# Performance work log

Hardware: AMD Instinct MI355X
Metric: run time of the kernel (lower is better)

The kernel has to match this reference:

```python
import jax, jax.numpy as jnp
import numpy as np

D_MODEL = 2048
N_HEADS = 16
N_KV_HEADS = 4
D_K = D_MODEL // N_HEADS          # 128
N_REP = N_HEADS // N_KV_HEADS     # 4
MAX_SEQ_LEN = 2048


def _rope_tables():
    # Matches torch Rotary: d_k//4 geometric freqs followed by d_k//4 zeros.
    freqs = (1.0 / 10000.0) ** jnp.linspace(0.0, 1.0, D_K // 4, dtype=jnp.float32)
    freqs = jnp.concatenate([freqs, jnp.zeros(D_K // 4, dtype=jnp.float32)])
    t = jnp.arange(MAX_SEQ_LEN, dtype=jnp.float32)
    theta = t[:, None] * freqs[None, :]          # [max_seq_len, d_k//2]
    return jnp.cos(theta), jnp.sin(theta)


def _apply_rotary(x, cos, sin):
    # Faithful to original: x is (B, H, T, D) and the table is indexed by
    # x.size(-3) == H (the original code rotates per-HEAD, broadcast over time).
    H = x.shape[1]
    c = cos[None, :H, None, :]
    s = sin[None, :H, None, :]
    xf = x.astype(jnp.float32)
    x1, x2 = jnp.split(xf, 2, axis=-1)
    y1 = x1 * c + x2 * s
    y2 = -x1 * s + x2 * c
    return jnp.concatenate([y1, y2], axis=-1).astype(x.dtype)


def setup_inputs() -> dict:
    key = jax.random.key(0)
    ks = jax.random.split(key, 5)
    B, T = 2, 2048
    scale = 1.0 / np.sqrt(D_MODEL)
    x = jax.random.normal(ks[0], (B, T, D_MODEL), dtype=jnp.float32)
    wq = jax.random.normal(ks[1], (N_HEADS * D_K, D_MODEL), dtype=jnp.float32) * scale
    wk = jax.random.normal(ks[2], (N_KV_HEADS * D_K, D_MODEL), dtype=jnp.float32) * scale
    wv = jax.random.normal(ks[3], (N_KV_HEADS * D_K, D_MODEL), dtype=jnp.float32) * scale
    wo = jax.random.normal(ks[4], (D_MODEL, D_MODEL), dtype=jnp.float32) * scale
    return {"x": x, "wq": wq, "wk": wk, "wv": wv, "wo": wo}


def reference(x, wq, wk, wv, wo):
    B, T, _ = x.shape
    cos, sin = _rope_tables()

    Q = (x @ wq.T).reshape(B, T, N_HEADS, D_K).transpose(0, 2, 1, 3)      # (B,Hq,T,D)
    K = (x @ wk.T).reshape(B, T, N_KV_HEADS, D_K).transpose(0, 2, 1, 3)   # (B,Hkv,T,D)
    V = (x @ wv.T).reshape(B, T, N_KV_HEADS, D_K).transpose(0, 2, 1, 3)

    Q = _apply_rotary(Q, cos, sin)
    K = _apply_rotary(K, cos, sin)

    # repeat_interleave over head dim to match query heads
    K = jnp.repeat(K, N_REP, axis=1)   # (B,Hq,T,D)
    V = jnp.repeat(V, N_REP, axis=1)

    scale = 1.0 / jnp.sqrt(jnp.asarray(D_K, dtype=jnp.float32))
    scores = jnp.einsum('bhqd,bhkd->bhqk', Q, K) * scale
    causal = jnp.tril(jnp.ones((T, T), dtype=bool))
    scores = jnp.where(causal[None, None, :, :], scores, jnp.finfo(scores.dtype).min)
    attn = jax.nn.softmax(scores, axis=-1)
    out = jnp.einsum('bhqk,bhkd->bhqd', attn, V)          # (B,Hq,T,D)
    out = out.transpose(0, 2, 1, 3).reshape(B, T, D_MODEL)
    return out @ wo.T
```

## Files before the change

### kernel.cpp

```cpp
#include <hip/hip_runtime.h>
#include <cstdint>
#include <cstddef>

typedef __attribute__((ext_vector_type(8))) short bf16x8;
typedef __attribute__((ext_vector_type(4))) float f32x4;
typedef __attribute__((ext_vector_type(16))) float f32x16;
typedef unsigned short ushort_t;

#define MFMA_BF16(a, b, c) __builtin_amdgcn_mfma_f32_16x16x32_bf16((a), (b), (c), 0, 0, 0)
#define MFMA32_BF16(a, b, c) __builtin_amdgcn_mfma_f32_32x32x16_bf16((a), (b), (c), 0, 0, 0)

__device__ __forceinline__ unsigned short f2bf(float f) {
  unsigned int u = __float_as_uint(f);
  u += 0x7fffu + ((u >> 16) & 1u);
  return (unsigned short)(u >> 16);
}
__device__ __forceinline__ float bf2f(unsigned short h) {
  return __uint_as_float(((unsigned int)h) << 16);
}
__device__ __forceinline__ float exp2_fast(float x) {
  float r;
  asm("v_exp_f32 %0, %1" : "=v"(r) : "v"(x));
  return r;
}
__device__ __forceinline__ uint32_t cvtpk_bf16(float lo, float hi) {
  uint32_t r;
  asm("v_cvt_pk_bf16_f32 %0, %1, %2" : "=v"(r) : "v"(lo), "v"(hi));
  return r;
}

__device__ __forceinline__ void gload_lds16(const void* g, void* lds) {
  __builtin_amdgcn_global_load_lds(
      (const __attribute__((address_space(1))) void*)g,
      (__attribute__((address_space(3))) void*)lds, 16, 0, 0);
}

__global__ __launch_bounds__(256)
void cvt_kernel(const float* __restrict__ x, const float* __restrict__ wq,
                const float* __restrict__ wk, const float* __restrict__ wv,
                const float* __restrict__ wo,
                ushort_t* __restrict__ xb, ushort_t* __restrict__ wqb,
                ushort_t* __restrict__ wkb, ushort_t* __restrict__ wvb,
                ushort_t* __restrict__ wob) {
  const float* src; ushort_t* dst; int n;
  switch (blockIdx.y) {
    case 0:  src = x;  dst = xb;  n = 8388608; break;
    case 1:  src = wq; dst = wqb; n = 4194304; break;
    case 2:  src = wk; dst = wkb; n = 1048576; break;
    case 3:  src = wv; dst = wvb; n = 1048576; break;
    default: src = wo; dst = wob; n = 4194304; break;
  }
  const int i = (int)(blockIdx.x * 256u + threadIdx.x) * 4;
  if (i >= n) return;
  const float4 v = *(const float4*)(src + i);
  union { unsigned short us[4]; unsigned long long u64; } pk;
  pk.us[0] = f2bf(v.x); pk.us[1] = f2bf(v.y);
  pk.us[2] = f2bf(v.z); pk.us[3] = f2bf(v.w);
  *(unsigned long long*)(dst + i) = pk.u64;
}

__global__ __launch_bounds__(256, 2)
void gemm_qkv(const ushort_t* __restrict__ A,
              const ushort_t* __restrict__ WQ, const ushort_t* __restrict__ WK,
              const ushort_t* __restrict__ WV,
              ushort_t* __restrict__ Qb, ushort_t* __restrict__ Kb,
              ushort_t* __restrict__ Vtb) {
  __shared__ bf16x8 smem_v[4096];
  char* smem = (char*)smem_v;
  const int tid  = threadIdx.x;
  const int lane = tid & 63;
  const int wave = tid >> 6;
  const int wr = wave >> 1, wc = wave & 1;
  const int y = blockIdx.y;
  int mode, ylocal;
  const ushort_t* Bsel;
  if (y < 16)      { mode = 0; ylocal = y;      Bsel = WQ; }
  else if (y < 20) { mode = 1; ylocal = y - 16; Bsel = WK; }
  else             { mode = 2; ylocal = y - 20; Bsel = WV; }
  const ushort_t* Abase = A + (size_t)blockIdx.x * 128 * 2048;
  const ushort_t* Bbase = Bsel + (size_t)ylocal * 128 * 2048;

  f32x4 acc[4][4] = {};

  #pragma unroll
  for (int it = 0; it < 4; ++it) {
    const int chunk = it * 4 + wave;
    const int r  = chunk * 8 + (lane >> 3);
    const int cg = (lane & 7) ^ (r & 7);
    gload_lds16(Abase + (size_t)r * 2048 + cg * 8, smem + chunk * 1024);
    gload_lds16(Bbase + (size_t)r * 2048 + cg * 8, smem + 16384 + chunk * 1024);
  }
  __syncthreads();

  for (int t = 0; t < 32; ++t) {
    if (t + 1 < 32) {
      char* dst = smem + ((t + 1) & 1) * 32768;
      const int k0 = (t + 1) * 64;
      #pragma unroll
      for (int it = 0; it < 4; ++it) {
        const int chunk = it * 4 + wave;
        const int r  = chunk * 8 + (lane >> 3);
        const int cg = (lane & 7) ^ (r & 7);
        gload_lds16(Abase + (size_t)r * 2048 + k0 + cg * 8, dst + chunk * 1024);
        gload_lds16(Bbase + (size_t)r * 2048 + k0 + cg * 8, dst + 16384 + chunk * 1024);
      }
    }

    char* As = smem + (t & 1) * 32768;
    char* Bs = As + 16384;
    bf16x8 af[2][4], bf_[2][4];
    #pragma unroll
    for (int kki = 0; kki < 2; ++kki) {
      #pragma unroll
      for (int m = 0; m < 4; ++m) {
        const int row = wr * 64 + m * 16 + (lane & 15);
        const int cg  = ((kki << 2) + (lane >> 4)) ^ (row & 7);
        af[kki][m] = *(const bf16x8*)(As + row * 128 + cg * 16);
      }
      #pragma unroll
      for (int n = 0; n < 4; ++n) {
        const int row = wc * 64 + n * 16 + (lane & 15);
        const int cg  = ((kki << 2) + (lane >> 4)) ^ (row & 7);
        bf_[kki][n] = *(const bf16x8*)(Bs + row * 128 + cg * 16);
      }
    }
    #pragma unroll
    for (int kki = 0; kki < 2; ++kki)
      #pragma unroll
      for (int m = 0; m < 4; ++m)
        #pragma unroll
        for (int n = 0; n < 4; ++n)
          acc[m][n] = MFMA_BF16(af[kki][m], bf_[kki][n], acc[m][n]);

    __syncthreads();
  }

  const int row0 = blockIdx.x * 128 + wr * 64;
  const int col0 = ylocal * 128 + wc * 64;
  #pragma unroll
  for (int m = 0; m < 4; ++m) {
    #pragma unroll
    for (int n = 0; n < 4; ++n) {
      #pragma unroll
      for (int j = 0; j < 4; ++j) {
        const int gm = row0 + m * 16 + ((lane >> 4) << 2) + j;
        const int gn = col0 + n * 16 + (lane & 15);
        const float v = acc[m][n][j];
        if (mode == 0) {
          Qb[(size_t)gm * 2048 + gn] = f2bf(v);
        } else if (mode == 1) {
          Kb[(size_t)gm * 512 + gn] = f2bf(v);
        } else {
          const int bb = gm >> 11, t2 = gm & 2047;
          Vtb[(size_t)bb * 512 * 2048 + (size_t)gn * 2048 + t2] = f2bf(v);
        }
      }
    }
  }
}

template<int WMODE>
__global__ __launch_bounds__(256, 2)
void gemm_bt(const ushort_t* __restrict__ A, const ushort_t* __restrict__ B,
             void* __restrict__ Cout, int M, int N, int K) {
  __shared__ bf16x8 smem_v[4096];
  char* smem = (char*)smem_v;
  const int tid  = threadIdx.x;
  const int lane = tid & 63;
  const int wave = tid >> 6;
  const int wr = wave >> 1, wc = wave & 1;
  const ushort_t* Abase = A + (size_t)blockIdx.x * 128 * K;
  const ushort_t* Bbase = B + (size_t)blockIdx.y * 128 * K;

  f32x4 acc[4][4] = {};
  const int nk = K >> 6;

  #pragma unroll
  for (int it = 0; it < 4; ++it) {
    const int chunk = it * 4 + wave;
    const int r  = chunk * 8 + (lane >> 3);
    const int cg = (lane & 7) ^ (r & 7);
    gload_lds16(Abase + (size_t)r * K + cg * 8, smem + chunk * 1024);
    gload_lds16(Bbase + (size_t)r * K + cg * 8, smem + 16384 + chunk * 1024);
  }
  __syncthreads();

  for (int t = 0; t < nk; ++t) {
    if (t + 1 < nk) {
      char* dst = smem + ((t + 1) & 1) * 32768;
      const int k0 = (t + 1) * 64;
      #pragma unroll
      for (int it = 0; it < 4; ++it) {
        const int chunk = it * 4 + wave;
        const int r  = chunk * 8 + (lane >> 3);
        const int cg = (lane & 7) ^ (r & 7);
        gload_lds16(Abase + (size_t)r * K + k0 + cg * 8, dst + chunk * 1024);
        gload_lds16(Bbase + (size_t)r * K + k0 + cg * 8, dst + 16384 + chunk * 1024);
      }
    }

    char* As = smem + (t & 1) * 32768;
    char* Bs = As + 16384;
    bf16x8 af[2][4], bf_[2][4];
    #pragma unroll
    for (int kki = 0; kki < 2; ++kki) {
      #pragma unroll
      for (int m = 0; m < 4; ++m) {
        const int row = wr * 64 + m * 16 + (lane & 15);
        const int cg  = ((kki << 2) + (lane >> 4)) ^ (row & 7);
        af[kki][m] = *(const bf16x8*)(As + row * 128 + cg * 16);
      }
      #pragma unroll
      for (int n = 0; n < 4; ++n) {
        const int row = wc * 64 + n * 16 + (lane & 15);
        const int cg  = ((kki << 2) + (lane >> 4)) ^ (row & 7);
        bf_[kki][n] = *(const bf16x8*)(Bs + row * 128 + cg * 16);
      }
    }
    #pragma unroll
    for (int kki = 0; kki < 2; ++kki)
      #pragma unroll
      for (int m = 0; m < 4; ++m)
        #pragma unroll
        for (int n = 0; n < 4; ++n)
          acc[m][n] = MFMA_BF16(af[kki][m], bf_[kki][n], acc[m][n]);

    __syncthreads();
  }

  const int row0 = blockIdx.x * 128 + wr * 64;
  const int col0 = blockIdx.y * 128 + wc * 64;
  #pragma unroll
  for (int m = 0; m < 4; ++m) {
    #pragma unroll
    for (int n = 0; n < 4; ++n) {
      #pragma unroll
      for (int j = 0; j < 4; ++j) {
        const int gm = row0 + m * 16 + ((lane >> 4) << 2) + j;
        const int gn = col0 + n * 16 + (lane & 15);
        const float v = acc[m][n][j];
        if (WMODE == 0) {
          ((ushort_t*)Cout)[(size_t)gm * N + gn] = f2bf(v);
        } else if (WMODE == 1) {
          ((float*)Cout)[(size_t)gm * N + gn] = v;
        } else {
          const int bb = gm >> 11, t2 = gm & 2047;
          ((ushort_t*)Cout)[(size_t)bb * N * 2048 + (size_t)gn * 2048 + t2] = f2bf(v);
        }
      }
    }
  }
}

__global__ __launch_bounds__(256)
void rope_k_kernel(ushort_t* __restrict__ K) {
  const int idx = blockIdx.x * 256 + threadIdx.x;
  const int NK = 4096 * 4 * 32;
  if (idx >= NK) return;
  const int t = idx >> 7, r = idx & 127;
  const int h = r >> 5, i = r & 31;
  ushort_t* p = K + (size_t)t * 512 + h * 128;
  const float f  = powf(10000.0f, -(float)i / 31.0f);
  const float th = (float)h * f;
  float sn, cs;
  sincosf(th, &sn, &cs);
  const float x1 = bf2f(p[i]), x2 = bf2f(p[i + 64]);
  p[i]      = f2bf(x1 * cs + x2 * sn);
  p[i + 64] = f2bf(-x1 * sn + x2 * cs);
}

__global__ __launch_bounds__(256, 2)
void attn_kernel(const ushort_t* __restrict__ Q, const ushort_t* __restrict__ K,
                 const ushort_t* __restrict__ Vt, ushort_t* __restrict__ AO) {
  __shared__ bf16x8 smem_v[4096];
  char* smem = (char*)smem_v;
  const int tid  = threadIdx.x;
  const int lane = tid & 63;
  const int wq   = tid >> 6;
  const int ql   = lane & 31;
  const int hi   = lane >> 5;
  const int h  = blockIdx.y;
  const int b  = blockIdx.z;
  const int qt = (b == 0) ? ((int)gridDim.x - 1 - (int)blockIdx.x)
                          : (int)blockIdx.x;
  const int kh = h >> 2;
  const int q0b = qt * 128;
  const int qmin_w = q0b + wq * 32;
  const int qmax_w = qmin_w + 31;
  const int qrow = qmin_w + ql;

  const ushort_t* Qp = Q  + (size_t)b * 2048 * 2048 + (size_t)h  * 128;
  const ushort_t* Kp = K  + (size_t)b * 2048 * 512  + (size_t)kh * 128;
  const ushort_t* Vp = Vt + (size_t)b * 512 * 2048  + (size_t)kh * 128 * 2048;

  const int ntiles = (qt + 1) * 2;

  #pragma unroll
  for (int it = 0; it < 4; ++it) {
    const int ck = it * 4 + wq;
    const int rK = ck * 4 + (lane >> 4);
    const int gK = (lane & 15) ^ (rK & 7);
    gload_lds16(Kp + (size_t)rK * 512 + gK * 8, smem + ck * 1024);
    const int rV = ck * 8 + (lane >> 3);
    const int gV = (lane & 7) ^ (rV & 7);
    gload_lds16(Vp + (size_t)rV * 2048 + gV * 8, smem + 16384 + ck * 1024);
  }

  const float SCL = 0.08838834764831845f * 1.4426950408889634f;
  bf16x8 qf[8];
  #pragma unroll
  for (int ks = 0; ks < 8; ++ks)
    qf[ks] = *(const bf16x8*)(Qp + (size_t)qrow * 2048 + ks * 16 + hi * 8);
  #pragma unroll
  for (int ks = 0; ks < 2; ++ks) {
    union { bf16x8 v; ushort_t us[8]; } X1, X2;
    X1.v = qf[ks]; X2.v = qf[ks + 4];
    #pragma unroll
    for (int e = 0; e < 8; ++e) {
      const int i = ks * 16 + hi * 8 + e;
      const float f = __expf(-(float)i * (9.2103403720f / 31.0f));
      float sn, cs;
      sincosf((float)h * f, &sn, &cs);
      const float x1 = bf2f(X1.us[e]), x2 = bf2f(X2.us[e]);
      X1.us[e] = f2bf((x1 * cs + x2 * sn) * SCL);
      X2.us[e] = f2bf((-x1 * sn + x2 * cs) * SCL);
    }
    qf[ks] = X1.v; qf[ks + 4] = X2.v;
  }
  #pragma unroll
  for (int ks = 2; ks < 4; ++ks) {
    union { bf16x8 v; ushort_t us[8]; } X1, X2;
    X1.v = qf[ks]; X2.v = qf[ks + 4];
    #pragma unroll
    for (int e = 0; e < 8; ++e) {
      X1.us[e] = f2bf(bf2f(X1.us[e]) * SCL);
      X2.us[e] = f2bf(bf2f(X2.us[e]) * SCL);
    }
    qf[ks] = X1.v; qf[ks + 4] = X2.v;
  }

  float m_ = -3.0e38f, l_ = 0.f;
  f32x16 oacc[4] = {};

  __syncthreads();

  for (int ti = 0; ti < ntiles; ++ti) {
    const int kv0 = ti * 64;
    if (ti + 1 < ntiles) {
      const int nkv0 = kv0 + 64;
      char* dst = smem + ((ti + 1) & 1) * 32768;
      #pragma unroll
      for (int it = 0; it < 4; ++it) {
        const int ck = it * 4 + wq;
        const int rK = ck * 4 + (lane >> 4);
        const int gK = (lane & 15) ^ (rK & 7);
        gload_lds16(Kp + (size_t)(nkv0 + rK) * 512 + gK * 8, dst + ck * 1024);
        const int rV = ck * 8 + (lane >> 3);
        const int gV = (lane & 7) ^ (rV & 7);
        gload_lds16(Vp + (size_t)rV * 2048 + nkv0 + gV * 8, dst + 16384 + ck * 1024);
      }
    }

    char* Ks = smem + (ti & 1) * 32768;
    char* Vs = Ks + 16384;
    if (kv0 <= qmax_w) {
      f32x16 sacc[2] = {};
      __builtin_amdgcn_s_setprio(1);
      #pragma unroll
      for (int kg = 0; kg < 2; ++kg) {
        const int key = kg * 32 + ql;
        #pragma unroll
        for (int ks = 0; ks < 8; ++ks) {
          const int g = ((ks << 1) + hi) ^ (key & 7);
          const bf16x8 kf = *(const bf16x8*)(Ks + key * 256 + g * 16);
          sacc[kg] = MFMA32_BF16(kf, qf[ks], sacc[kg]);
        }
      }
      __builtin_amdgcn_s_setprio(0);

      if (kv0 + 63 > qmin_w) {
        #pragma unroll
        for (int kg = 0; kg < 2; ++kg)
          #pragma unroll
          for (int r = 0; r < 16; ++r) {
            const int keyg = kv0 + kg * 32 + (r & 3) + 8 * (r >> 2) + 4 * hi;
            if (keyg > qrow) sacc[kg][r] = -3.0e38f;
          }
      }

      float mx[8];
      #pragma unroll
      for (int i = 0; i < 8; ++i) {
        const int kg = i >> 2, base = (i & 3) * 4;
        mx[i] = fmaxf(fmaxf(sacc[kg][base], sacc[kg][base + 1]),
                      fmaxf(sacc[kg][base + 2], sacc[kg][base + 3]));
      }
      float pm = fmaxf(fmaxf(fmaxf(mx[0], mx[1]), fmaxf(mx[2], mx[3])),
                       fmaxf(fmaxf(mx[4], mx[5]), fmaxf(mx[6], mx[7])));
      pm = fmaxf(pm, __shfl_xor(pm, 32));

      if (__any(pm > m_ + 11.0f)) {
        const float mn = fmaxf(m_, pm);
        const float alpha = exp2_fast(m_ - mn);
        m_ = mn;
        l_ *= alpha;
        #pragma unroll
        for (int r = 0; r < 16; ++r) {
          const float ar = __shfl(alpha, (r & 3) + 8 * (r >> 2) + 4 * hi);
          #pragma unroll
          for (int dg = 0; dg < 4; ++dg) oacc[dg][r] *= ar;
        }
      }

      float rs0 = 0.f, rs1 = 0.f, rs2 = 0.f, rs3 = 0.f;
      #pragma unroll
      for (int kg = 0; kg < 2; ++kg)
        #pragma unroll
        for (int r = 0; r < 16; r += 4) {
          const float p0 = exp2_fast(sacc[kg][r]     - m_);
          const float p1 = exp2_fast(sacc[kg][r + 1] - m_);
          const float p2 = exp2_fast(sacc[kg][r + 2] - m_);
          const float p3 = exp2_fast(sacc[kg][r + 3] - m_);
          sacc[kg][r] = p0; sacc[kg][r + 1] = p1;
          sacc[kg][r + 2] = p2; sacc[kg][r + 3] = p3;
          rs0 += p0; rs1 += p1; rs2 += p2; rs3 += p3;
        }
      float rs = (rs0 + rs1) + (rs2 + rs3);
      rs += __shfl_xor(rs, 32);
      l_ += rs;

      bf16x8 pa[4];
      #pragma unroll
      for (int ks = 0; ks < 4; ++ks) {
        const int kg = ks >> 1;
        const int base = 8 * (ks & 1);
        union { uint32_t w[4]; bf16x8 v; } U;
        #pragma unroll
        for (int j = 0; j < 2; ++j) {
          uint32_t a  = cvtpk_bf16(sacc[kg][base + 2 * j],     sacc[kg][base + 2 * j + 1]);
          uint32_t bb = cvtpk_bf16(sacc[kg][base + 4 + 2 * j], sacc[kg][base + 4 + 2 * j + 1]);
          asm volatile("v_permlane32_swap_b32 %0, %1" : "+v"(a), "+v"(bb));
          U.w[j] = a; U.w[2 + j] = bb;
        }
        pa[ks] = U.v;
      }

      __builtin_amdgcn_s_setprio(1);
      #pragma unroll
      for (int dg = 0; dg < 4; ++dg) {
        const int d = dg * 32 + ql;
        #pragma unroll
        for (int ks = 0; ks < 4; ++ks) {
          const int g = ((ks << 1) + hi) ^ (d & 7);
          const bf16x8 vf = *(const bf16x8*)(Vs + d * 128 + g * 16);
          oacc[dg] = MFMA32_BF16(pa[ks], vf, oacc[dg]);
        }
      }
      __builtin_amdgcn_s_setprio(0);
    }

    __syncthreads();
  }

  const float linv = 1.0f / l_;
  ushort_t* AOp = AO + (size_t)b * 2048 * 2048 + (size_t)h * 128;
  #pragma unroll
  for (int r = 0; r < 16; ++r) {
    const int cr = (r & 3) + 8 * (r >> 2) + 4 * hi;
    const float li = __shfl(linv, cr);
    const int row = q0b + wq * 32 + cr;
    #pragma unroll
    for (int dg = 0; dg < 4; ++dg)
      AOp[(size_t)row * 2048 + dg * 32 + ql] = f2bf(oacc[dg][r] * li);
  }
}

extern "C" void kernel_launch(void* const* d_in, const int* in_sizes, int n_in,
                              void* d_out, int out_size, void* d_ws, size_t ws_size,
                              hipStream_t stream) {
  const float* x  = (const float*)d_in[0];
  const float* wq = (const float*)d_in[1];
  const float* wk = (const float*)d_in[2];
  const float* wv = (const float*)d_in[3];
  const float* wo = (const float*)d_in[4];
  float* out = (float*)d_out;
  char* ws = (char*)d_ws;

  ushort_t* xb  = (ushort_t*)(ws);
  ushort_t* wqb = (ushort_t*)(ws + 16777216);
  ushort_t* wkb = (ushort_t*)(ws + 25165824);
  ushort_t* wvb = (ushort_t*)(ws + 27262976);
  ushort_t* wob = (ushort_t*)(ws + 29360128);
  ushort_t* Qb  = (ushort_t*)(ws + 37748736);
  ushort_t* Kb  = (ushort_t*)(ws + 54525952);
  ushort_t* Vtb = (ushort_t*)(ws + 58720256);
  ushort_t* AOb = (ushort_t*)(ws + 62914560);

  cvt_kernel<<<dim3(8192, 5), 256, 0, stream>>>(x, wq, wk, wv, wo,
                                                xb, wqb, wkb, wvb, wob);
  gemm_qkv<<<dim3(32, 24), 256, 0, stream>>>(xb, wqb, wkb, wvb, Qb, Kb, Vtb);
  rope_k_kernel<<<dim3(2048), 256, 0, stream>>>(Kb);
  attn_kernel<<<dim3(16, 16, 2), 256, 0, stream>>>(Qb, Kb, Vtb, AOb);
  gemm_bt<1><<<dim3(32, 16), 256, 0, stream>>>(AOb, wob, out, 4096, 2048, 2048);
}
```

Baseline: 189.9 us.

## Remap attention blocks to XCDs by KV head and prefetch V fragments early

Block indices are remapped so that all blocks sharing a batch and KV head land on the same XCD. The goal is better L2 reuse of K/V across the four query heads that share them. Causal load balancing is kept by pairing short and long q tiles. Per-lane K/V load offsets are now computed once and reused in every prefetch, and V fragments are read from LDS before the softmax so their latency overlaps with it. The cost is 16 more bf16x8 registers per lane, which may pressure the 2-blocks-per-SM occupancy target.

```diff
diff --git a/kernel.cpp b/kernel.cpp
--- a/kernel.cpp
+++ b/kernel.cpp
@@ -279,11 +279,16 @@
   const int wq   = tid >> 6;
   const int ql   = lane & 31;
   const int hi   = lane >> 5;
-  const int h  = blockIdx.y;
-  const int b  = blockIdx.z;
-  const int qt = (b == 0) ? ((int)gridDim.x - 1 - (int)blockIdx.x)
-                          : (int)blockIdx.x;
-  const int kh = h >> 2;
+
+  const int lin = (int)blockIdx.x + 16 * (int)blockIdx.y + 256 * (int)blockIdx.z;
+  const int xcd = lin & 7;
+  const int s   = lin >> 3;
+  const int b   = xcd >> 2;
+  const int kh  = xcd & 3;
+  const int h   = (kh << 2) + (s & 3);
+  const int s4  = s >> 2;
+  const int qt  = (s4 < 8) ? s4 : (23 - s4);
+
   const int q0b = qt * 128;
   const int qmin_w = q0b + wq * 32;
   const int qmax_w = qmin_w + 31;
@@ -295,15 +300,22 @@
 
   const int ntiles = (qt + 1) * 2;
 
+  int offK[4], offV[4], ldK[4], ldV[4];
   #pragma unroll
   for (int it = 0; it < 4; ++it) {
     const int ck = it * 4 + wq;
     const int rK = ck * 4 + (lane >> 4);
     const int gK = (lane & 15) ^ (rK & 7);
-    gload_lds16(Kp + (size_t)rK * 512 + gK * 8, smem + ck * 1024);
+    offK[it] = rK * 512 + gK * 8;  ldK[it] = ck * 1024;
     const int rV = ck * 8 + (lane >> 3);
     const int gV = (lane & 7) ^ (rV & 7);
-    gload_lds16(Vp + (size_t)rV * 2048 + gV * 8, smem + 16384 + ck * 1024);
+    offV[it] = rV * 2048 + gV * 8; ldV[it] = 16384 + ck * 1024;
+  }
+
+  #pragma unroll
+  for (int it = 0; it < 4; ++it) {
+    gload_lds16(Kp + offK[it], smem + ldK[it]);
+    gload_lds16(Vp + offV[it], smem + ldV[it]);
   }
 
   const float SCL = 0.08838834764831845f * 1.4426950408889634f;
@@ -347,17 +359,13 @@
   for (int ti = 0; ti < ntiles; ++ti) {
     const int kv0 = ti * 64;
     if (ti + 1 < ntiles) {
-      const int nkv0 = kv0 + 64;
+      const ushort_t* Kt = Kp + (size_t)(kv0 + 64) * 512;
+      const ushort_t* Vn = Vp + (kv0 + 64);
       char* dst = smem + ((ti + 1) & 1) * 32768;
       #pragma unroll
       for (int it = 0; it < 4; ++it) {
-        const int ck = it * 4 + wq;
-        const int rK = ck * 4 + (lane >> 4);
-        const int gK = (lane & 15) ^ (rK & 7);
-        gload_lds16(Kp + (size_t)(nkv0 + rK) * 512 + gK * 8, dst + ck * 1024);
-        const int rV = ck * 8 + (lane >> 3);
-        const int gV = (lane & 7) ^ (rV & 7);
-        gload_lds16(Vp + (size_t)rV * 2048 + nkv0 + gV * 8, dst + 16384 + ck * 1024);
+        gload_lds16(Kt + offK[it], dst + ldK[it]);
+        gload_lds16(Vn + offV[it], dst + ldV[it]);
       }
     }
 
@@ -377,6 +385,17 @@
         }
       }
       __builtin_amdgcn_s_setprio(0);
+
+      bf16x8 vfr[4][4];
+      #pragma unroll
+      for (int dg = 0; dg < 4; ++dg) {
+        const int d = dg * 32 + ql;
+        #pragma unroll
+        for (int ks = 0; ks < 4; ++ks) {
+          const int g = ((ks << 1) + hi) ^ (d & 7);
+          vfr[dg][ks] = *(const bf16x8*)(Vs + d * 128 + g * 16);
+        }
+      }
 
       if (kv0 + 63 > qmin_w) {
         #pragma unroll
@@ -447,15 +466,10 @@
 
       __builtin_amdgcn_s_setprio(1);
       #pragma unroll
-      for (int dg = 0; dg < 4; ++dg) {
-        const int d = dg * 32 + ql;
-        #pragma unroll
-        for (int ks = 0; ks < 4; ++ks) {
-          const int g = ((ks << 1) + hi) ^ (d & 7);
-          const bf16x8 vf = *(const bf16x8*)(Vs + d * 128 + g * 16);
-          oacc[dg] = MFMA32_BF16(pa[ks], vf, oacc[dg]);
-        }
-      }
+      for (int dg = 0; dg < 4; ++dg)
+        #pragma unroll
+        for (int ks = 0; ks < 4; ++ks)
+          oacc[dg] = MFMA32_BF16(pa[ks], vfr[dg][ks], oacc[dg]);
       __builtin_amdgcn_s_setprio(0);
     }
 
```

Result: no change. 187.6 us (-1.2%).
